# Kernel optimization log

Hardware: AMD Instinct MI355X
Metric: run time of the kernel (lower is better)

Reference implementation:

```python
import jax, jax.numpy as jnp
import numpy as np

LAM_S = 0.7
LAM_L = 0.3
ANCHOR_PAGES = 4
FLOW_WINDOW = 8
FLASH_TOP_K = 32
Q_MAX = 32
NEG = -10000.0


def setup_inputs() -> dict:
    B, N, P, Dp = 8, 1024, 64, 1024
    L = N * P
    key = jax.random.key(0)
    ks = jax.random.split(key, 9)
    block_repr = jax.random.normal(ks[0], (B, N, Dp), jnp.float32)
    query_hidden = jax.random.normal(ks[1], (B, Dp), jnp.float32)
    input_ids = jax.random.randint(ks[2], (B, L), 0, 32000, jnp.int32)
    token_level_weights = jax.random.uniform(ks[3], (B, L), jnp.float32)
    token_valid = jnp.ones((B, L), bool)
    page_valid = jax.random.uniform(ks[4], (B, N, P)) < 0.97
    page_indices = jnp.broadcast_to(jnp.arange(L, dtype=jnp.int32).reshape(1, N, P), (B, N, P))
    token2page = jnp.broadcast_to((jnp.arange(L, dtype=jnp.int32) // P)[None, :], (B, L))
    segment_ids = jax.random.randint(ks[5], (B, N), 0, 4, jnp.int32)
    query_pos = jax.random.randint(ks[6], (B,), L // 2, L, jnp.int32)
    query_start = jax.random.randint(ks[7], (B,), 0, L - Q_MAX, jnp.int32)
    query_end = query_start + jax.random.randint(ks[8], (B,), 0, Q_MAX, jnp.int32)
    return dict(block_repr=block_repr, query_hidden=query_hidden, query_pos=query_pos,
                input_ids=input_ids, token_level_weights=token_level_weights,
                query_start=query_start, query_end=query_end, segment_ids=segment_ids,
                page_valid=page_valid, page_indices=page_indices,
                token2page=token2page, token_valid=token_valid)


def _l2norm(x):
    # F.normalize: x / max(||x||, eps)
    return x / jnp.maximum(jnp.linalg.norm(x, axis=-1, keepdims=True), 1e-12)


def _norm_scores(scores, mask):
    # per-batch min-max normalization over masked entries, 0 elsewhere
    v_min = jnp.where(mask, scores, jnp.inf).min(axis=1, keepdims=True)
    v_max = jnp.where(mask, scores, -jnp.inf).max(axis=1, keepdims=True)
    rng = v_max - v_min
    flat = rng < 1e-6  # includes empty-mask rows (rng = -inf)
    normed = jnp.where(flat, 0.0, (scores - v_min) / jnp.where(flat, 1.0, rng))
    return jnp.where(mask, normed, 0.0)


def reference(block_repr, query_hidden, query_pos, input_ids, token_level_weights,
              query_start, query_end, segment_ids, page_valid, page_indices,
              token2page, token_valid):
    B, N, Dp = block_repr.shape
    L = input_ids.shape[1]
    P = page_valid.shape[2]

    # ---- semantic scores (single query vector path) ----
    k_vec = _l2norm(block_repr)                       # [B,N,Dp]
    q_vec = _l2norm(query_hidden)                     # [B,Dp]
    scores_sem = jnp.einsum('bd,bnd->bn', q_vec, k_vec)

    # ---- lexical scores ----
    qs = jnp.clip(query_start, 0, L - 1)
    qe = jnp.clip(query_end, 0, L - 1)
    j = jnp.arange(Q_MAX, dtype=jnp.int32)
    pos = jnp.clip(qs[:, None] + j[None, :], 0, L - 1)            # [B,Q]
    qmask = (j[None, :] <= (qe - qs)[:, None]) & (query_end >= query_start)[:, None]
    qmask = qmask & jnp.take_along_axis(token_valid, pos, axis=1)
    q_ids = jnp.where(qmask, jnp.take_along_axis(input_ids, pos, axis=1), -1)  # [B,Q], -1 never matches

    idx_flat = page_indices.reshape(B, N * P)
    tok = jnp.take_along_axis(input_ids, idx_flat, axis=1).reshape(B, N, P)
    w_page = jnp.take_along_axis(token_level_weights, idx_flat, axis=1).reshape(B, N, P)
    in_q = (tok[..., None] == q_ids[:, None, None, :]).any(-1)    # [B,N,P] isin
    scores_lex = jnp.where(page_valid & in_q, w_page, 0.0).sum(-1)  # [B,N]

    # ---- masks ----
    query_page = jnp.clip(jnp.take_along_axis(token2page, query_pos[:, None], axis=1)[:, 0], 0)
    page_idx = jnp.arange(N, dtype=jnp.int32)[None, :]
    valid_mask = page_valid.any(-1) & (segment_ids >= 0) & (page_idx <= query_page[:, None])

    sem_n = _norm_scores(scores_sem, valid_mask)
    lex_n = _norm_scores(scores_lex, valid_mask)
    scores_mix = (LAM_S * sem_n + LAM_L * lex_n) / (LAM_S + LAM_L)
    scores_final = jnp.where(valid_mask, scores_mix, NEG)

    # ---- keep-page selection ----
    is_seg0 = (segment_ids == 0) & valid_mask
    anchor = is_seg0 & (jnp.cumsum(is_seg0, axis=1) <= ANCHOR_PAGES)
    lower = jnp.clip(query_page - FLOW_WINDOW, 0)
    flow = (page_idx >= lower[:, None]) & (page_idx <= query_page[:, None]) & valid_mask
    flow = flow.at[jnp.arange(B), query_page].set(True)
    base_keep = anchor | flow
    candidate = valid_mask & ~base_keep
    scores_candidate = jnp.where(candidate, scores_final, NEG)
    k = min(FLASH_TOP_K, N)
    _, topk_idx = jax.lax.top_k(scores_candidate, k)
    flash = jnp.zeros_like(candidate).at[jnp.arange(B)[:, None], topk_idx].set(True) & candidate
    return base_keep | flash
```

## Files before the change

kernel.cpp:

```cpp
#include <hip/hip_runtime.h>
#include <hip/hip_bf16.h>
#include <cstdint>
#include <cstddef>

#define LAM_S_F 0.7f
#define LAM_L_F 0.3f
#define ANCHOR_PAGES 4
#define FLOW_WINDOW 8
#define FLASH_TOP_K 32
#define QMAX 32
#define NEGF (-10000.0f)

__device__ __forceinline__ float wave_sum(float v) {
#pragma unroll
  for (int off = 32; off > 0; off >>= 1) v += __shfl_xor(v, off);
  return v;
}

__global__ __launch_bounds__(256) void qp_scores_kernel(
    const float* __restrict__ block_repr,
    const float* __restrict__ query_hidden,
    const int*   __restrict__ input_ids,
    const float* __restrict__ tok_w,
    const int*   __restrict__ query_start,
    const int*   __restrict__ query_end,
    const int*   __restrict__ page_valid,
    const int*   __restrict__ page_indices,
    const int*   __restrict__ token_valid,
    float* __restrict__ o_sem,
    float* __restrict__ o_lex,
    int*   __restrict__ o_pany,
    int N, int P, int Dp, int L)
{
  const int n   = blockIdx.x;
  const int b   = blockIdx.y;
  const int tid = threadIdx.x;

  __shared__ int   qids[QMAX];
  __shared__ float part[4][3];

  if (tid < QMAX) {
    const int qsr = query_start[b], qer = query_end[b];
    const int qs = min(max(qsr, 0), L - 1);
    const int qe = min(max(qer, 0), L - 1);
    const int pos = min(qs + tid, L - 1);
    const bool m = (tid <= qe - qs) && (qer >= qsr) &&
                   (token_valid[(size_t)b * L + pos] != 0);
    qids[tid] = m ? input_ids[(size_t)b * L + pos] : -1;
  }

  const float4 kv =
      reinterpret_cast<const float4*>(block_repr + ((size_t)b * N + n) * Dp)[tid];
  const float4 qv =
      reinterpret_cast<const float4*>(query_hidden + (size_t)b * Dp)[tid];
  float s_qk = kv.x * qv.x + kv.y * qv.y + kv.z * qv.z + kv.w * qv.w;
  float s_kk = kv.x * kv.x + kv.y * kv.y + kv.z * kv.z + kv.w * kv.w;
  float s_qq = qv.x * qv.x + qv.y * qv.y + qv.z * qv.z + qv.w * qv.w;

  __syncthreads();

  float lex = 0.f;
  bool  pv  = false;
  if (tid < P) {
    const size_t pbase = ((size_t)b * N + n) * (size_t)P + tid;
    const int   idx = page_indices[pbase];
    pv              = (page_valid[pbase] != 0);
    const int   tk  = input_ids[(size_t)b * L + idx];
    const float w   = tok_w[(size_t)b * L + idx];
    bool match = false;
#pragma unroll
    for (int q = 0; q < QMAX; ++q) match = match || (tk == qids[q]);
    lex = (pv && match) ? w : 0.f;
  }

  s_qk = wave_sum(s_qk);
  s_kk = wave_sum(s_kk);
  s_qq = wave_sum(s_qq);
  const int lane = tid & 63, wid = tid >> 6;
  if (lane == 0) { part[wid][0] = s_qk; part[wid][1] = s_kk; part[wid][2] = s_qq; }

  float lexs = 0.f;
  unsigned long long anyv = 0ull;
  if (wid == 0) {
    lexs = wave_sum(lex);
    anyv = __ballot(pv);
  }
  __syncthreads();

  if (tid == 0) {
    const float S1 = part[0][0] + part[1][0] + part[2][0] + part[3][0];
    const float S2 = part[0][1] + part[1][1] + part[2][1] + part[3][1];
    const float S3 = part[0][2] + part[1][2] + part[2][2] + part[3][2];
    const float sem =
        S1 / (fmaxf(sqrtf(S3), 1e-12f) * fmaxf(sqrtf(S2), 1e-12f));
    const size_t o = (size_t)b * N + n;
    o_sem[o]  = sem;
    o_lex[o]  = lexs;
    o_pany[o] = (anyv != 0ull) ? 1 : 0;
  }
}

__global__ __launch_bounds__(1024) void qp_select_kernel(
    const float* __restrict__ o_sem,
    const float* __restrict__ o_lex,
    const int*   __restrict__ o_pany,
    const int*   __restrict__ segment_ids,
    const int*   __restrict__ token2page,
    const int*   __restrict__ query_pos,
    int* __restrict__ out,
    int N, int L)
{
  const int b    = blockIdx.x;
  const int n    = threadIdx.x;
  const int lane = n & 63;
  const int wid  = n >> 6;
  const int NW   = blockDim.x >> 6;

  __shared__ float sc_arr[1024];
  __shared__ unsigned char fl_arr[1024];
  __shared__ float wred[16][4];
  __shared__ int   wcnt[16];
  __shared__ float g[4];

  const int qp = max(token2page[(size_t)b * L + (size_t)query_pos[b]], 0);
  const size_t o = (size_t)b * N + n;
  const float sem = o_sem[o];
  const float lex = o_lex[o];
  const int   seg = segment_ids[o];
  const bool  valid = (o_pany[o] != 0) && (seg >= 0) && (n <= qp);

  float smin = valid ? sem : INFINITY;
  float smax = valid ? sem : -INFINITY;
  float lmin = valid ? lex : INFINITY;
  float lmax = valid ? lex : -INFINITY;
#pragma unroll
  for (int off = 32; off > 0; off >>= 1) {
    smin = fminf(smin, __shfl_xor(smin, off));
    smax = fmaxf(smax, __shfl_xor(smax, off));
    lmin = fminf(lmin, __shfl_xor(lmin, off));
    lmax = fmaxf(lmax, __shfl_xor(lmax, off));
  }

  const bool is0 = (seg == 0) && valid;
  const unsigned long long bal = __ballot(is0);
  const int excl = (int)__popcll(bal & ((1ull << lane) - 1ull));

  if (lane == 0) {
    wred[wid][0] = smin; wred[wid][1] = smax;
    wred[wid][2] = lmin; wred[wid][3] = lmax;
    wcnt[wid] = (int)__popcll(bal);
  }
  __syncthreads();

  if (n == 0) {
    float a = INFINITY, bmx = -INFINITY, c = INFINITY, d = -INFINITY;
    for (int w = 0; w < NW; ++w) {
      a   = fminf(a, wred[w][0]);
      bmx = fmaxf(bmx, wred[w][1]);
      c   = fminf(c, wred[w][2]);
      d   = fmaxf(d, wred[w][3]);
    }
    g[0] = a; g[1] = bmx; g[2] = c; g[3] = d;
  }
  int prior = 0;
  for (int w = 0; w < wid; ++w) prior += wcnt[w];
  __syncthreads();

  const int  cum    = prior + excl + (is0 ? 1 : 0);
  const bool anchor = is0 && (cum <= ANCHOR_PAGES);

  const float rng_s = g[1] - g[0];
  const float rng_l = g[3] - g[2];
  const float sem_n = (rng_s < 1e-6f) ? 0.f : (sem - g[0]) / rng_s;
  const float lex_n = (rng_l < 1e-6f) ? 0.f : (lex - g[2]) / rng_l;
  const float mix = (LAM_S_F * sem_n + LAM_L_F * lex_n) / (LAM_S_F + LAM_L_F);

  const int  lower = max(qp - FLOW_WINDOW, 0);
  const bool flow  = ((n >= lower) && (n <= qp) && valid) || (n == qp);
  const bool base_keep = anchor || flow;
  const bool cand = valid && !base_keep;

  sc_arr[n] = cand ? mix : NEGF;
  fl_arr[n] = 0;
  __syncthreads();

  if (wid == 0) {
    float bestv = -INFINITY;
    int   besti = lane;
#pragma unroll
    for (int i = 0; i < 16; ++i) {
      const int idx = lane + (i << 6);
      const float v = sc_arr[idx];
      if (v > bestv) { bestv = v; besti = idx; }
    }
    for (int t = 0; t < FLASH_TOP_K; ++t) {
      float v = bestv;
      int   ix = besti;
#pragma unroll
      for (int off = 1; off < 64; off <<= 1) {
        const float ov  = __shfl_xor(v, off);
        const int   oix = __shfl_xor(ix, off);
        if (ov > v || (ov == v && oix < ix)) { v = ov; ix = oix; }
      }
      if (!(v > NEGF + 1.0f)) break;
      if ((ix & 63) == lane) {
        fl_arr[ix] = 1;
        sc_arr[ix] = -INFINITY;
        bestv = -INFINITY; besti = lane;
#pragma unroll
        for (int i = 0; i < 16; ++i) {
          const int idx = lane + (i << 6);
          const float vv = sc_arr[idx];
          if (vv > bestv) { bestv = vv; besti = idx; }
        }
      }
    }
  }
  __syncthreads();

  out[o] = (base_keep || (fl_arr[n] != 0)) ? 1 : 0;
}

extern "C" void kernel_launch(void* const* d_in, const int* in_sizes, int n_in,
                              void* d_out, int out_size, void* d_ws, size_t ws_size,
                              hipStream_t stream) {
  const float* block_repr   = (const float*)d_in[0];
  const float* query_hidden = (const float*)d_in[1];
  const int*   query_pos    = (const int*)d_in[2];
  const int*   input_ids    = (const int*)d_in[3];
  const float* tok_w        = (const float*)d_in[4];
  const int*   query_start  = (const int*)d_in[5];
  const int*   query_end    = (const int*)d_in[6];
  const int*   segment_ids  = (const int*)d_in[7];
  const int*   page_valid   = (const int*)d_in[8];
  const int*   page_indices = (const int*)d_in[9];
  const int*   token2page   = (const int*)d_in[10];
  const int*   token_valid  = (const int*)d_in[11];

  const int B  = in_sizes[2];
  const int Dp = in_sizes[1] / B;
  const int L  = in_sizes[3] / B;
  const int N  = in_sizes[7] / B;
  const int P  = in_sizes[8] / (B * N);

  float* o_sem  = (float*)d_ws;
  float* o_lex  = o_sem + (size_t)B * N;
  int*   o_pany = (int*)(o_lex + (size_t)B * N);
  int*   out    = (int*)d_out;

  dim3 g1(N, B);
  qp_scores_kernel<<<g1, dim3(256), 0, stream>>>(
      block_repr, query_hidden, input_ids, tok_w, query_start, query_end,
      page_valid, page_indices, token_valid, o_sem, o_lex, o_pany, N, P, Dp, L);

  qp_select_kernel<<<dim3(B), dim3(N), 0, stream>>>(
      o_sem, o_lex, o_pany, segment_ids, token2page, query_pos, out, N, L);
}
```

Before: 131.6 us.

## Skip score computation for pages beyond query page; pack top-k keys

The scoring kernel now reads the query page up front and exits early for pages past it, so their block_repr rows and token data are never loaded. The select kernel no longer stores floats in shared memory and rescans them each round. It packs each candidate's score bits and inverted index into a 64-bit key held in registers, so each top-k round is a register max plus a wave reduction. This trades extra per-block index loads for skipping invalid pages, and relies on mix being non-negative for the bit ordering.

```diff
diff --git a/kernel.cpp b/kernel.cpp
--- a/kernel.cpp
+++ b/kernel.cpp
@@ -27,6 +27,8 @@
     const int*   __restrict__ page_valid,
     const int*   __restrict__ page_indices,
     const int*   __restrict__ token_valid,
+    const int*   __restrict__ token2page,
+    const int*   __restrict__ query_pos,
     float* __restrict__ o_sem,
     float* __restrict__ o_lex,
     int*   __restrict__ o_pany,
@@ -35,6 +37,15 @@
   const int n   = blockIdx.x;
   const int b   = blockIdx.y;
   const int tid = threadIdx.x;
+
+  const int qp = max(token2page[(size_t)b * L + (size_t)query_pos[b]], 0);
+  if (n > qp) {
+    if (tid == 0) {
+      const size_t o = (size_t)b * N + n;
+      o_sem[o] = 0.f; o_lex[o] = 0.f; o_pany[o] = 0;
+    }
+    return;
+  }
 
   __shared__ int   qids[QMAX];
   __shared__ float part[4][3];
@@ -116,7 +127,7 @@
   const int wid  = n >> 6;
   const int NW   = blockDim.x >> 6;
 
-  __shared__ float sc_arr[1024];
+  __shared__ unsigned long long key_arr[1024];
   __shared__ unsigned char fl_arr[1024];
   __shared__ float wred[16][4];
   __shared__ int   wcnt[16];
@@ -180,39 +191,32 @@
   const bool base_keep = anchor || flow;
   const bool cand = valid && !base_keep;
 
-  sc_arr[n] = cand ? mix : NEGF;
+  const unsigned int sb = __float_as_uint(mix);
+  key_arr[n] = cand
+      ? ((((unsigned long long)(sb + 1u)) << 10) | (unsigned long long)(1023 - n))
+      : 0ull;
   fl_arr[n] = 0;
   __syncthreads();
 
   if (wid == 0) {
-    float bestv = -INFINITY;
-    int   besti = lane;
-#pragma unroll
-    for (int i = 0; i < 16; ++i) {
-      const int idx = lane + (i << 6);
-      const float v = sc_arr[idx];
-      if (v > bestv) { bestv = v; besti = idx; }
-    }
+    unsigned long long kk[16];
+#pragma unroll
+    for (int i = 0; i < 16; ++i) kk[i] = key_arr[lane + (i << 6)];
     for (int t = 0; t < FLASH_TOP_K; ++t) {
-      float v = bestv;
-      int   ix = besti;
+      unsigned long long lm = 0ull;
+#pragma unroll
+      for (int i = 0; i < 16; ++i) lm = (kk[i] > lm) ? kk[i] : lm;
 #pragma unroll
       for (int off = 1; off < 64; off <<= 1) {
-        const float ov  = __shfl_xor(v, off);
-        const int   oix = __shfl_xor(ix, off);
-        if (ov > v || (ov == v && oix < ix)) { v = ov; ix = oix; }
+        const unsigned long long ov = __shfl_xor(lm, off);
+        lm = (ov > lm) ? ov : lm;
       }
-      if (!(v > NEGF + 1.0f)) break;
-      if ((ix & 63) == lane) {
-        fl_arr[ix] = 1;
-        sc_arr[ix] = -INFINITY;
-        bestv = -INFINITY; besti = lane;
-#pragma unroll
-        for (int i = 0; i < 16; ++i) {
-          const int idx = lane + (i << 6);
-          const float vv = sc_arr[idx];
-          if (vv > bestv) { bestv = vv; besti = idx; }
-        }
+      if (lm == 0ull) break;
+      const int win = 1023 - (int)(lm & 1023ull);
+      if ((win & 63) == lane) {
+        fl_arr[win] = 1;
+#pragma unroll
+        for (int i = 0; i < 16; ++i) if (i == (win >> 6)) kk[i] = 0ull;
       }
     }
   }
@@ -251,7 +255,8 @@
   dim3 g1(N, B);
   qp_scores_kernel<<<g1, dim3(256), 0, stream>>>(
       block_repr, query_hidden, input_ids, tok_w, query_start, query_end,
-      page_valid, page_indices, token_valid, o_sem, o_lex, o_pany, N, P, Dp, L);
+      page_valid, page_indices, token_valid, token2page, query_pos,
+      o_sem, o_lex, o_pany, N, P, Dp, L);
 
   qp_select_kernel<<<dim3(B), dim3(N), 0, stream>>>(
       o_sem, o_lex, o_pany, segment_ids, token2page, query_pos, out, N, L);
```

Result: faster. 125.7 us (-4.5%).
